# Optimization experiments

Hardware: AMD Instinct MI355X
Metric: run time of the kernel (lower is better)

The kernel has to match this reference:

```python
import jax, jax.numpy as jnp
import numpy as np

B, N, C = 64, 197, 768
H = 12
D = C // H
SCALE = D ** -0.5
TAU = 5.0
THRESHOLD = 0.6
NEG_INF = float('-inf')


def setup_inputs() -> dict:
    key = jax.random.key(0)
    ks = jax.random.split(key, 10)
    def gumbel(k, shape):
        # -log(Exponential) == standard Gumbel noise, matches torch exponential_().log()
        e = jax.random.exponential(k, shape, dtype=jnp.float32)
        return -jnp.log(e + 1e-10)
    s = 0.02
    return {
        'x': jax.random.normal(ks[0], (B, N, C), dtype=jnp.float32),
        'g1': gumbel(ks[1], (B, N - 1, 1)),
        'g2': gumbel(ks[2], (B, N - 1, 1)),
        'Wq': jax.random.normal(ks[3], (C, C), dtype=jnp.float32) * s,
        'Wk': jax.random.normal(ks[4], (C, C), dtype=jnp.float32) * s,
        'Wv': jax.random.normal(ks[5], (C, C), dtype=jnp.float32) * s,
        'Wp': jax.random.normal(ks[6], (C, C), dtype=jnp.float32) * s,
        'bp': jnp.zeros((C,), dtype=jnp.float32),
        'Wm': jax.random.normal(ks[7], (1, C), dtype=jnp.float32) * s,
        'bm': jnp.zeros((1,), dtype=jnp.float32),
    }


def reference(x, g1, g2, Wq, Wk, Wv, Wp, bp, Wm, bm):
    b, n, c = x.shape
    # QKV projections (qkv_bias=False), reshape to (B, H, N, D)
    q = (x @ Wq.T).reshape(b, n, H, D).transpose(0, 2, 1, 3)
    k = (x @ Wk.T).reshape(b, n, H, D).transpose(0, 2, 1, 3)
    v = (x @ Wv.T).reshape(b, n, H, D).transpose(0, 2, 1, 3)

    attn_pre = jnp.einsum('bhnd,bhmd->bhnm', q, k) * SCALE  # (B,H,N,N)

    # SimpleTokenSelect: gumbel-sigmoid gating on non-CLS tokens (training=True, hard=True)
    logits = x[:, 1:] @ Wm.T + bm                       # (B, N-1, 1)
    y_soft = jax.nn.sigmoid((logits + g1 - g2) / TAU)
    y_hard = (y_soft > THRESHOLD).astype(y_soft.dtype)
    ts = y_hard - jax.lax.stop_gradient(y_soft) + y_soft  # straight-through
    ts = jnp.concatenate([jnp.ones((b, 1, 1), dtype=ts.dtype), ts], axis=1)[..., 0]  # (B, N)

    # attention policy = outer product of token gates, detached (ada_token_detach_attn)
    policy = jax.lax.stop_gradient(jnp.einsum('bn,bm->bnm', ts, ts))[:, None]  # (B,1,N,N)

    # pre-softmax masking: zero gated scores, -inf off-diagonal entries of gated rows
    eye = jnp.eye(n, dtype=attn_pre.dtype)
    neg_mask = jnp.where(1.0 - policy - eye > 0, NEG_INF, 0.0)
    attn = jax.nn.softmax(attn_pre * policy + neg_mask, axis=-1)

    out = jnp.einsum('bhnm,bhmd->bhnd', attn, v)        # (B,H,N,D)
    out = out.transpose(0, 2, 1, 3).reshape(b, n, c)
    out = out @ Wp.T + bp                                # proj (dropout p=0)
    return out
```

## Files before the change

kernel.cpp:

```cpp
#include <hip/hip_runtime.h>
#include <hip/hip_bf16.h>
#include <cstdint>

typedef unsigned short u16;
typedef __attribute__((ext_vector_type(8))) short bf16x8;
typedef __attribute__((ext_vector_type(4))) float f32x4;

#define NB 64
#define NN 197
#define NC 768
#define NH 12
#define ND 64
#define NM (NB*NN)
#define CAP 96
#define NT 24
#define SELR 6144
#define MSELT 48
#define ASZ ((size_t)NM*NC)
#define WSZ ((size_t)NC*NC)
#define SELSZ2 ((size_t)SELR*NC)

__device__ __forceinline__ u16 f2bf(float f) {
  uint32_t u = __float_as_uint(f);
  u += 0x7fffu + ((u >> 16) & 1u);
  return (u16)(u >> 16);
}

__device__ __forceinline__ void gl_lds16(const u16* g, u16* l) {
  __builtin_amdgcn_global_load_lds(
      (const __attribute__((address_space(1))) void*)g,
      (__attribute__((address_space(3))) void*)l, 16, 0, 0);
}

#define GATEB 3152
#define WBLK 576
#define TRBLK 144
__global__ __launch_bounds__(256) void k1_prep(const float* __restrict__ x,
    const float* __restrict__ g1, const float* __restrict__ g2,
    const float* __restrict__ Wm, const float* __restrict__ bm,
    const float* __restrict__ wq, const float* __restrict__ wk,
    const float* __restrict__ wv, const float* __restrict__ wp,
    u16* __restrict__ xb, u16* __restrict__ wqb, u16* __restrict__ wkb,
    u16* __restrict__ wvb, u16* __restrict__ wpb, u16* __restrict__ wvt,
    float* __restrict__ ts) {
  __shared__ u16 T[64][72];
  int bid = blockIdx.x, tid = threadIdx.x;

  if (bid < GATEB) {
    int wave = tid >> 6, lane = tid & 63;
    int wid = bid * 4 + wave;
    int b = wid / NN, n = wid % NN;
    const float* xr = x + (size_t)wid * NC;
    u16* xbr = xb + (size_t)wid * NC;
    double acc = 0.0;
    #pragma unroll
    for (int i = 0; i < 3; ++i) {
      float4 f = *(const float4*)(xr + lane * 4 + 256 * i);
      float4 w = *(const float4*)(Wm + lane * 4 + 256 * i);
      acc += (double)f.x * w.x + (double)f.y * w.y
           + (double)f.z * w.z + (double)f.w * w.w;
      ushort4 o;
      o.x = f2bf(f.x); o.y = f2bf(f.y); o.z = f2bf(f.z); o.w = f2bf(f.w);
      *(ushort4*)(xbr + lane * 4 + 256 * i) = o;
    }
    #pragma unroll
    for (int off = 32; off; off >>= 1) acc += __shfl_down(acc, off);
    float o = 1.0f;
    if (n != 0) {
      double z = (acc + (double)bm[0] + (double)g1[b*(NN-1) + n - 1]
                                      - (double)g2[b*(NN-1) + n - 1]) / 5.0;
      o = (z > 0.4054651081081643820) ? 1.0f : 0.0f;
    }
    if (lane == 0) ts[wid] = o;
    return;
  }
  bid -= GATEB;
  if (bid < 4*WBLK) {
    int seg = bid / WBLK;
    int i = (bid - seg * WBLK) * 256 + tid;
    const float* src; u16* dst;
    if (seg == 0)      { src = wq; dst = wqb; }
    else if (seg == 1) { src = wk; dst = wkb; }
    else if (seg == 2) { src = wv; dst = wvb; }
    else               { src = wp; dst = wpb; }
    float4 f = ((const float4*)src)[i];
    ushort4 o;
    o.x = f2bf(f.x); o.y = f2bf(f.y); o.z = f2bf(f.z); o.w = f2bf(f.w);
    ((ushort4*)dst)[i] = o;
    return;
  }
  bid -= 4*WBLK;
  {
    int bx = bid % 12, by = bid / 12;
    int j0 = by * 64, k0 = bx * 64;
    #pragma unroll
    for (int g = 0; g < 4; ++g) {
      int r = g * 16 + (tid >> 4);
      int c4 = (tid & 15) * 4;
      float4 f = *(const float4*)(wv + (size_t)(j0 + r) * NC + k0 + c4);
      T[c4 + 0][r] = f2bf(f.x);
      T[c4 + 1][r] = f2bf(f.y);
      T[c4 + 2][r] = f2bf(f.z);
      T[c4 + 3][r] = f2bf(f.w);
    }
    __syncthreads();
    #pragma unroll
    for (int g = 0; g < 4; ++g) {
      int r = g * 16 + (tid >> 4);
      int c4 = (tid & 15) * 4;
      ushort4 o = *(ushort4*)&T[r][c4];
      *(ushort4*)(wvt + (size_t)(k0 + r) * NC + j0 + c4) = o;
    }
  }
}

__global__ __launch_bounds__(1024) void ck_compact(const float* __restrict__ ts,
    int* __restrict__ cnt, int* __restrict__ boff, int* __restrict__ gidx) {
  __shared__ unsigned long long masks[NB][4];
  __shared__ int scnt[NB];
  __shared__ int soff[NB + 1];
  int tid = threadIdx.x, lane = tid & 63, wave = tid >> 6;

  #pragma unroll
  for (int p = 0; p < 4; ++p) {
    int b = wave * 4 + p;
    int count = 0;
    #pragma unroll
    for (int c = 0; c < 4; ++c) {
      int t = c * 64 + lane;
      bool sel = (t < NN) && (ts[b * NN + t] > 0.5f);
      unsigned long long m = __ballot(sel);
      if (lane == 0) masks[b][c] = m;
      count += __popcll(m);
    }
    if (lane == 0) scnt[b] = count < CAP ? count : CAP;
  }
  __syncthreads();

  if (wave == 0) {
    int acc = 0;
    for (int i = 0; i < NB; ++i) {
      int v = scnt[i];
      if (i < lane) acc += v;
    }
    soff[lane] = acc;
    if (lane == 63) soff[NB] = acc + scnt[63];
  }
  __syncthreads();

  #pragma unroll
  for (int p = 0; p < 4; ++p) {
    int b = wave * 4 + p;
    int base = soff[b];
    int cc = scnt[b];
    int prior = 0;
    #pragma unroll
    for (int c = 0; c < 4; ++c) {
      unsigned long long m = masks[b][c];
      int t = c * 64 + lane;
      bool sel = ((m >> lane) & 1ull) != 0;
      int within = __popcll(m & ((lane == 0) ? 0ull : (~0ull >> (64 - lane))));
      int pos = prior + within;
      if (sel && pos < cc) gidx[base + pos] = b * NN + t;
      prior += __popcll(m);
    }
  }
  if (tid < NB) { cnt[tid] = scnt[tid]; boff[tid] = soff[tid]; }
  if (tid == NB) boff[NB] = soff[NB];
  __syncthreads();
  int total = soff[NB];
  for (int i = total + tid; i < SELR; i += 1024) gidx[i] = 0;
}

__global__ __launch_bounds__(256) void k2_wvp_qkv(const u16* __restrict__ xb,
    const u16* __restrict__ wq3, const u16* __restrict__ wpb,
    const u16* __restrict__ wvt, u16* __restrict__ wvpb,
    u16* __restrict__ sel3, const int* __restrict__ boff,
    const int* __restrict__ gidx) {
  alignas(16) __shared__ u16 SA[128][32];
  alignas(16) __shared__ u16 SB[128][32];
  int bid = blockIdx.x;
  int tid = threadIdx.x, lane = tid & 63, wave = tid >> 6;
  int lr = lane & 15, lg = lane >> 4, lk = lg * 8;
  int wr = (wave >> 1) * 64, wc = (wave & 1) * 64;

  int id0 = (wave*2 + 0) * 64 + lane, id1 = (wave*2 + 1) * 64 + lane;
  const u16 *baseA0, *baseA1, *baseB0, *baseB1;
  bool isSel = (bid < MSELT * 18);
  int m0, n0, total = 0, z = 0;
  if (isSel) {
    int mt = bid / 18, r18 = bid % 18;
    z = r18 / 6; int y = r18 % 6;
    total = boff[NB];
    m0 = mt * 128;
    if (m0 >= total) return;
    n0 = y * 128;
    const u16* W = wq3 + (size_t)z * WSZ;
    baseA0 = xb + (size_t)gidx[m0 + (id0 >> 2)] * NC + (id0 & 3) * 8;
    baseA1 = xb + (size_t)gidx[m0 + (id1 >> 2)] * NC + (id1 & 3) * 8;
    baseB0 = W + (size_t)(n0 + (id0 >> 2)) * NC + (id0 & 3) * 8;
    baseB1 = W + (size_t)(n0 + (id1 >> 2)) * NC + (id1 & 3) * 8;
  } else {
    int wb = bid - MSELT * 18;
    m0 = (wb / 6) * 128; n0 = (wb % 6) * 128;
    baseA0 = wpb + (size_t)(m0 + (id0 >> 2)) * NC + (id0 & 3) * 8;
    baseA1 = wpb + (size_t)(m0 + (id1 >> 2)) * NC + (id1 & 3) * 8;
    baseB0 = wvt + (size_t)(n0 + (id0 >> 2)) * NC + (id0 & 3) * 8;
    baseB1 = wvt + (size_t)(n0 + (id1 >> 2)) * NC + (id1 & 3) * 8;
  }
  u16* dA0 = &SA[0][0] + (size_t)(wave*2 + 0) * 512;
  u16* dA1 = &SA[0][0] + (size_t)(wave*2 + 1) * 512;
  u16* dB0 = &SB[0][0] + (size_t)(wave*2 + 0) * 512;
  u16* dB1 = &SB[0][0] + (size_t)(wave*2 + 1) * 512;

  f32x4 acc[4][4];
  #pragma unroll
  for (int i = 0; i < 4; ++i)
    #pragma unroll
    for (int j = 0; j < 4; ++j) acc[i][j] = (f32x4){0.f,0.f,0.f,0.f};

  for (int k0 = 0; k0 < NC; k0 += 32) {
    gl_lds16(baseA0 + k0, dA0);
    gl_lds16(baseA1 + k0, dA1);
    gl_lds16(baseB0 + k0, dB0);
    gl_lds16(baseB1 + k0, dB1);
    __syncthreads();
    bf16x8 af[4], bfr[4];
    #pragma unroll
    for (int f = 0; f < 4; ++f) {
      af[f]  = *(const bf16x8*)(&SA[wr + f*16 + lr][lk]);
      bfr[f] = *(const bf16x8*)(&SB[wc + f*16 + lr][lk]);
    }
    #pragma unroll
    for (int i = 0; i < 4; ++i)
      #pragma unroll
      for (int j = 0; j < 4; ++j)
        acc[i][j] = __builtin_amdgcn_mfma_f32_16x16x32_bf16(af[i], bfr[j], acc[i][j], 0, 0, 0);
    __syncthreads();
  }

  if (isSel) {
    u16* o = sel3 + (size_t)z * SELSZ2;
    #pragma unroll
    for (int i = 0; i < 4; ++i) {
      int rbase = m0 + wr + i*16 + 4*lg;
      #pragma unroll
      for (int j = 0; j < 4; ++j) {
        int col = n0 + wc + j*16 + lr;
        #pragma unroll
        for (int r = 0; r < 4; ++r) {
          int row = rbase + r;
          if (row < total)
            o[(size_t)row * NC + col] = f2bf(acc[i][j][r]);
        }
      }
    }
  } else {
    #pragma unroll
    for (int i = 0; i < 4; ++i)
      #pragma unroll
      for (int j = 0; j < 4; ++j)
        #pragma unroll
        for (int r = 0; r < 4; ++r)
          wvpb[(size_t)(m0 + wr + i*16 + 4*lg + r) * NC + n0 + wc + j*16 + lr] =
              f2bf(acc[i][j][r]);
  }
}

#define DTOT 594
#define DN1 378
#define DN2 (DTOT-DN1)
__global__ __launch_bounds__(256) void k3_dense_attn(const u16* __restrict__ xb,
    const u16* __restrict__ wvpb, const u16* __restrict__ qsel,
    const u16* __restrict__ ksel, const u16* __restrict__ vsel,
    u16* __restrict__ zsel, const float* __restrict__ ts,
    const float* __restrict__ bp, float* __restrict__ out,
    const int* __restrict__ cnt, const int* __restrict__ boff) {
  alignas(16) __shared__ u16 LDSU[64*232];
  int bid = blockIdx.x;
  int tid = threadIdx.x, lane = tid & 63, wave = tid >> 6;
  int lr = lane & 15, lg = lane >> 4;

  if (bid < DN1) {
    u16 (*SA)[32] = reinterpret_cast<u16(*)[32]>(&LDSU[0]);
    u16 (*SB)[32] = reinterpret_cast<u16(*)[32]>(&LDSU[4096]);
    int lk = lg * 8;
    int wr = (wave >> 1) * 64, wc = (wave & 1) * 64;
    int d = bid;
    int xcd = d & 7, loc = d >> 3;
    int wgid = (xcd < 2 ? xcd * 75 : 150 + (xcd - 2) * 74) + loc;
    int m0 = (wgid / 6) * 128, n0 = (wgid % 6) * 128;

    int id0 = (wave*2 + 0) * 64 + lane, id1 = (wave*2 + 1) * 64 + lane;
    const u16* baseA0 = xb + (size_t)(m0 + (id0 >> 2)) * NC + (id0 & 3) * 8;
    const u16* baseA1 = xb + (size_t)(m0 + (id1 >> 2)) * NC + (id1 & 3) * 8;
    const u16* baseB0 = wvpb + (size_t)(n0 + (id0 >> 2)) * NC + (id0 & 3) * 8;
    const u16* baseB1 = wvpb + (size_t)(n0 + (id1 >> 2)) * NC + (id1 & 3) * 8;
    u16* dA0 = &SA[0][0] + (size_t)(wave*2 + 0) * 512;
    u16* dA1 = &SA[0][0] + (size_t)(wave*2 + 1) * 512;
    u16* dB0 = &SB[0][0] + (size_t)(wave*2 + 0) * 512;
    u16* dB1 = &SB[0][0] + (size_t)(wave*2 + 1) * 512;

    f32x4 acc[4][4];
    #pragma unroll
    for (int i = 0; i < 4; ++i)
      #pragma unroll
      for (int j = 0; j < 4; ++j) acc[i][j] = (f32x4){0.f,0.f,0.f,0.f};

    for (int k0 = 0; k0 < NC; k0 += 32) {
      gl_lds16(baseA0 + k0, dA0);
      gl_lds16(baseA1 + k0, dA1);
      gl_lds16(baseB0 + k0, dB0);
      gl_lds16(baseB1 + k0, dB1);
      __syncthreads();
      bf16x8 af[4], bfr[4];
      #pragma unroll
      for (int f = 0; f < 4; ++f) {
        af[f]  = *(const bf16x8*)(&SA[wr + f*16 + lr][lk]);
        bfr[f] = *(const bf16x8*)(&SB[wc + f*16 + lr][lk]);
      }
      #pragma unroll
      for (int i = 0; i < 4; ++i)
        #pragma unroll
        for (int j = 0; j < 4; ++j)
          acc[i][j] = __builtin_amdgcn_mfma_f32_16x16x32_bf16(af[i], bfr[j], acc[i][j], 0, 0, 0);
      __syncthreads();
    }
    #pragma unroll
    for (int i = 0; i < 4; ++i) {
      int rbase = m0 + wr + i*16 + 4*lg;
      #pragma unroll
      for (int j = 0; j < 4; ++j) {
        int col = n0 + wc + j*16 + lr;
        #pragma unroll
        for (int r = 0; r < 4; ++r) {
          int row = rbase + r;
          if (row < NM && ts[row] < 0.5f)
            out[(size_t)row * NC + col] = acc[i][j][r] + bp[col];
        }
      }
    }
    return;
  }

  u16 (*Vt)[232] = reinterpret_cast<u16(*)[232]>(&LDSU[0]);
  int bh = bid - DN1;
  int b = bh / NH, h = bh % NH;
  int cntb = cnt[b];
  int boffb = boff[b];
  const size_t qbase = (size_t)boffb * NC + (size_t)h * ND;

  for (int id = tid; id < cntb * 8; id += 256) {
    int i = id >> 3, c8 = (id & 7) * 8;
    int4 val = *(const int4*)(vsel + qbase + (size_t)i * NC + c8);
    u16 tmp[8];
    *(int4*)tmp = val;
    #pragma unroll
    for (int e = 0; e < 8; ++e) Vt[c8 + e][i] = tmp[e];
  }
  for (int id = tid; id < 64 * 32; id += 256)
    Vt[id >> 5][cntb + (id & 31)] = 0;
  __syncthreads();

  int nchunk = (cntb + 15) >> 4;
  int mtmax  = nchunk;
  int mcmax  = (cntb + 31) >> 5;
  int idx0 = (((lane & 15) | ((lane & 16) << 1))) << 2;
  int idx1 = idx0 + 64;

  for (int qc = wave; qc < nchunk; qc += 4) {
    const u16* qp = qsel + qbase + (size_t)(qc * 16 + lr) * NC + lg * 8;
    bf16x8 qf0 = *(const bf16x8*)(qp);
    bf16x8 qf1 = *(const bf16x8*)(qp + 32);

    f32x4 s[6];
    #pragma unroll
    for (int mt = 0; mt < 6; ++mt) s[mt] = (f32x4){0.f,0.f,0.f,0.f};
    #pragma unroll
    for (int mt = 0; mt < 6; ++mt) {
      if (mt < mtmax) {
        const u16* kp = ksel + qbase + (size_t)(mt * 16 + lr) * NC + lg * 8;
        bf16x8 kf0 = *(const bf16x8*)(kp);
        bf16x8 kf1 = *(const bf16x8*)(kp + 32);
        f32x4 a = (f32x4){0.f,0.f,0.f,0.f};
        a = __builtin_amdgcn_mfma_f32_16x16x32_bf16(kf0, qf0, a, 0, 0, 0);
        a = __builtin_amdgcn_mfma_f32_16x16x32_bf16(kf1, qf1, a, 0, 0, 0);
        s[mt] = a;
      }
    }

    float mx = -3e38f;
    #pragma unroll
    for (int mt = 0; mt < 6; ++mt)
      #pragma unroll
      for (int jj = 0; jj < 4; ++jj) {
        int mm = mt*16 + 4*lg + jj;
        float val = (mm < cntb) ? s[mt][jj] * 0.125f : -1e30f;
        s[mt][jj] = val;
        mx = fmaxf(mx, val);
      }
    mx = fmaxf(mx, __shfl_xor(mx, 16));
    mx = fmaxf(mx, __shfl_xor(mx, 32));
    float sum = 0.f;
    #pragma unroll
    for (int mt = 0; mt < 6; ++mt)
      #pragma unroll
      for (int jj = 0; jj < 4; ++jj) {
        float pv = __expf(s[mt][jj] - mx);
        s[mt][jj] = pv;
        sum += pv;
      }
    sum += __shfl_xor(sum, 16);
    sum += __shfl_xor(sum, 32);
    float inv = 1.0f / sum;

    uint32_t u[6][2];
    #pragma unroll
    for (int mt = 0; mt < 6; ++mt) {
      u[mt][0] = ((uint32_t)f2bf(s[mt][1]*inv) << 16) | f2bf(s[mt][0]*inv);
      u[mt][1] = ((uint32_t)f2bf(s[mt][3]*inv) << 16) | f2bf(s[mt][2]*inv);
    }

    f32x4 oacc[4];
    #pragma unroll
    for (int dt = 0; dt < 4; ++dt) oacc[dt] = (f32x4){0.f,0.f,0.f,0.f};
    #pragma unroll
    for (int mc = 0; mc < 3; ++mc) {
      if (mc < mcmax) {
        uint32_t a0 = (uint32_t)__builtin_amdgcn_ds_bpermute(idx0, (int)u[2*mc][0]);
        uint32_t b0 = (uint32_t)__builtin_amdgcn_ds_bpermute(idx0, (int)u[2*mc+1][0]);
        uint32_t a1 = (uint32_t)__builtin_amdgcn_ds_bpermute(idx0, (int)u[2*mc][1]);
        uint32_t b1 = (uint32_t)__builtin_amdgcn_ds_bpermute(idx0, (int)u[2*mc+1][1]);
        uint32_t a2 = (uint32_t)__builtin_amdgcn_ds_bpermute(idx1, (int)u[2*mc][0]);
        uint32_t b2 = (uint32_t)__builtin_amdgcn_ds_bpermute(idx1, (int)u[2*mc+1][0]);
        uint32_t a3 = (uint32_t)__builtin_amdgcn_ds_bpermute(idx1, (int)u[2*mc][1]);
        uint32_t b3 = (uint32_t)__builtin_amdgcn_ds_bpermute(idx1, (int)u[2*mc+1][1]);
        bool hi = (lg >= 2);
        union { uint32_t w[4]; bf16x8 v; } pu;
        pu.w[0] = hi ? b0 : a0;
        pu.w[1] = hi ? b1 : a1;
        pu.w[2] = hi ? b2 : a2;
        pu.w[3] = hi ? b3 : a3;
        bf16x8 pa = pu.v;
        #pragma unroll
        for (int dt = 0; dt < 4; ++dt) {
          bf16x8 vf = *(const bf16x8*)(&Vt[dt*16 + lr][mc*32 + lg*8]);
          oacc[dt] = __builtin_amdgcn_mfma_f32_16x16x32_bf16(pa, vf, oacc[dt], 0, 0, 0);
        }
      }
    }

    #pragma unroll
    for (int r = 0; r < 4; ++r) {
      int nloc = qc*16 + 4*lg + r;
      if (nloc < cntb) {
        u16* op = zsel + qbase + (size_t)nloc * NC + lr;
        #pragma unroll
        for (int dt = 0; dt < 4; ++dt)
          op[dt*16] = f2bf(oacc[dt][r]);
      }
    }
  }
}

#define PJBLK (MSELT*6)
__global__ __launch_bounds__(256) void k4_out(const u16* __restrict__ xb,
    const u16* __restrict__ wvpb, const u16* __restrict__ zsel,
    const u16* __restrict__ wpb, const float* __restrict__ ts,
    const float* __restrict__ bp, float* __restrict__ out,
    const int* __restrict__ boff, const int* __restrict__ gidx) {
  alignas(16) __shared__ u16 SA[128][32];
  alignas(16) __shared__ u16 SB[128][32];
  int bid = blockIdx.x;
  int tid = threadIdx.x, lane = tid & 63, wave = tid >> 6;
  int lr = lane & 15, lg = lane >> 4, lk = lg * 8;
  int wr = (wave >> 1) * 64, wc = (wave & 1) * 64;

  const u16* Abase; const u16* Bbase;
  int m0, n0, total = 0;
  bool dense = (bid >= PJBLK);
  if (dense) {
    int d = DN1 + (bid - PJBLK);
    int xcd = d & 7, loc = d >> 3;
    int wgid = (xcd < 2 ? xcd * 75 : 150 + (xcd - 2) * 74) + loc;
    m0 = (wgid / 6) * 128;
    n0 = (wgid % 6) * 128;
    Abase = xb; Bbase = wvpb;
  } else {
    int mt = bid / 6, y = bid % 6;
    total = boff[NB];
    m0 = mt * 128;
    if (m0 >= total) return;
    n0 = y * 128;
    Abase = zsel; Bbase = wpb;
  }

  int id0 = (wave*2 + 0) * 64 + lane, id1 = (wave*2 + 1) * 64 + lane;
  const u16* baseA0 = Abase + (size_t)(m0 + (id0 >> 2)) * NC + (id0 & 3) * 8;
  const u16* baseA1 = Abase + (size_t)(m0 + (id1 >> 2)) * NC + (id1 & 3) * 8;
  const u16* baseB0 = Bbase + (size_t)(n0 + (id0 >> 2)) * NC + (id0 & 3) * 8;
  const u16* baseB1 = Bbase + (size_t)(n0 + (id1 >> 2)) * NC + (id1 & 3) * 8;
  u16* dA0 = &SA[0][0] + (size_t)(wave*2 + 0) * 512;
  u16* dA1 = &SA[0][0] + (size_t)(wave*2 + 1) * 512;
  u16* dB0 = &SB[0][0] + (size_t)(wave*2 + 0) * 512;
  u16* dB1 = &SB[0][0] + (size_t)(wave*2 + 1) * 512;

  f32x4 acc[4][4];
  #pragma unroll
  for (int i = 0; i < 4; ++i)
    #pragma unroll
    for (int j = 0; j < 4; ++j) acc[i][j] = (f32x4){0.f,0.f,0.f,0.f};

  for (int k0 = 0; k0 < NC; k0 += 32) {
    gl_lds16(baseA0 + k0, dA0);
    gl_lds16(baseA1 + k0, dA1);
    gl_lds16(baseB0 + k0, dB0);
    gl_lds16(baseB1 + k0, dB1);
    __syncthreads();
    bf16x8 af[4], bfr[4];
    #pragma unroll
    for (int f = 0; f < 4; ++f) {
      af[f]  = *(const bf16x8*)(&SA[wr + f*16 + lr][lk]);
      bfr[f] = *(const bf16x8*)(&SB[wc + f*16 + lr][lk]);
    }
    #pragma unroll
    for (int i = 0; i < 4; ++i)
      #pragma unroll
      for (int j = 0; j < 4; ++j)
        acc[i][j] = __builtin_amdgcn_mfma_f32_16x16x32_bf16(af[i], bfr[j], acc[i][j], 0, 0, 0);
    __syncthreads();
  }

  if (dense) {
    #pragma unroll
    for (int i = 0; i < 4; ++i) {
      int rbase = m0 + wr + i*16 + 4*lg;
      #pragma unroll
      for (int j = 0; j < 4; ++j) {
        int col = n0 + wc + j*16 + lr;
        #pragma unroll
        for (int r = 0; r < 4; ++r) {
          int row = rbase + r;
          if (row < NM && ts[row] < 0.5f)
            out[(size_t)row * NC + col] = acc[i][j][r] + bp[col];
        }
      }
    }
  } else {
    #pragma unroll
    for (int i = 0; i < 4; ++i) {
      int rbase = m0 + wr + i*16 + 4*lg;
      #pragma unroll
      for (int j = 0; j < 4; ++j) {
        int col = n0 + wc + j*16 + lr;
        #pragma unroll
        for (int r = 0; r < 4; ++r) {
          int row = rbase + r;
          if (row < total) {
            int grow = gidx[row];
            out[(size_t)grow * NC + col] = acc[i][j][r] + bp[col];
          }
        }
      }
    }
  }
}

extern "C" void kernel_launch(void* const* d_in, const int* in_sizes, int n_in,
                              void* d_out, int out_size, void* d_ws, size_t ws_size,
                              hipStream_t stream) {
  const float* x  = (const float*)d_in[0];
  const float* g1 = (const float*)d_in[1];
  const float* g2 = (const float*)d_in[2];
  const float* Wq = (const float*)d_in[3];
  const float* Wk = (const float*)d_in[4];
  const float* Wv = (const float*)d_in[5];
  const float* Wp = (const float*)d_in[6];
  const float* bp = (const float*)d_in[7];
  const float* Wm = (const float*)d_in[8];
  const float* bm = (const float*)d_in[9];
  float* out = (float*)d_out;

  const size_t act_sz = ASZ * 2;
  const size_t w_sz   = WSZ * 2;
  const size_t sel_sz = SELSZ2 * 2;
  size_t need = act_sz + 4*sel_sz + 6*w_sz + (size_t)NM*4
              + (size_t)(NB+1)*4 + (size_t)NB*4 + (size_t)SELR*4 + 256;
  if (ws_size < need) return;

  char* p = (char*)d_ws;
  u16* xb   = (u16*)p; p += act_sz;
  u16* qsel = (u16*)p; p += sel_sz;
  u16* ksel = (u16*)p; p += sel_sz;
  u16* vsel = (u16*)p; p += sel_sz;
  u16* zsel = (u16*)p; p += sel_sz;
  u16* wqb  = (u16*)p; p += w_sz;
  u16* wkb  = (u16*)p; p += w_sz;
  u16* wvb  = (u16*)p; p += w_sz;
  u16* wpb  = (u16*)p; p += w_sz;
  u16* wvtb = (u16*)p; p += w_sz;
  u16* wvpb = (u16*)p; p += w_sz;
  float* ts = (float*)p; p += (size_t)NM*4;
  int* cnt  = (int*)p;  p += (size_t)NB*4;
  int* boff = (int*)p;  p += (size_t)(NB+1)*4;
  int* gidx = (int*)p;
  (void)wkb; (void)wvb;

  k1_prep<<<dim3(GATEB + 4*WBLK + TRBLK), 256, 0, stream>>>(
      x, g1, g2, Wm, bm, Wq, Wk, Wv, Wp,
      xb, wqb, wkb, wvb, wpb, wvtb, ts);

  ck_compact<<<dim3(1), 1024, 0, stream>>>(ts, cnt, boff, gidx);

  k2_wvp_qkv<<<dim3(MSELT*18 + 36), 256, 0, stream>>>(
      xb, wqb, wpb, wvtb, wvpb, qsel, boff, gidx);

  k3_dense_attn<<<dim3(DN1 + NB*NH), 256, 0, stream>>>(
      xb, wvpb, qsel, ksel, vsel, zsel, ts, bp, out, cnt, boff);

  k4_out<<<dim3(PJBLK + DN2), 256, 0, stream>>>(
      xb, wvpb, zsel, wpb, ts, bp, out, boff, gidx);
}
```

Measured before the change: 113.0 us.

## Switch GEMMs to 256x128 tiles with 512-thread blocks via shared template body

Unifies the four GEMM paths into one templated body that computes 256x128 output tiles with 8 waves per block, replacing the 128x128 tiles with 4 waves. Each block now loads a taller A tile against the same B tile, halving B reloads per output and halving the block count. The dense/split partition counts and XCD remapping are retuned, and the attention part now runs with 8 waves per block. Fewer, larger blocks may reduce occupancy and worsen wave quantization on the CUs.

```diff
diff --git a/kernel.cpp b/kernel.cpp
--- a/kernel.cpp
+++ b/kernel.cpp
@@ -15,7 +15,7 @@
 #define CAP 96
 #define NT 24
 #define SELR 6144
-#define MSELT 48
+#define MT256 24
 #define ASZ ((size_t)NM*NC)
 #define WSZ ((size_t)NC*NC)
 #define SELSZ2 ((size_t)SELR*NC)
@@ -30,6 +30,80 @@
   __builtin_amdgcn_global_load_lds(
       (const __attribute__((address_space(1))) void*)g,
       (__attribute__((address_space(3))) void*)l, 16, 0, 0);
+}
+
+template<int GATHER, int OUTM>
+__device__ __forceinline__ void gemm256_body(
+    const u16* __restrict__ A, const u16* __restrict__ B,
+    u16* __restrict__ obf, float* __restrict__ of32,
+    const float* __restrict__ bias, const float* __restrict__ ts,
+    const int* __restrict__ gidx, int m0, int n0, int bound,
+    u16* SAf, u16* SBf) {
+  int tid = threadIdx.x, lane = tid & 63, wave = tid >> 6;
+  int lr = lane & 15, lg = lane >> 4, lk = lg * 8;
+  int wr = (wave >> 1) * 64, wc = (wave & 1) * 64;
+  int idA0 = tid, idA1 = 512 + tid, idB = tid;
+  const u16 *baseA0, *baseA1;
+  if (GATHER) {
+    baseA0 = A + (size_t)gidx[m0 + (idA0 >> 2)] * NC + (idA0 & 3) * 8;
+    baseA1 = A + (size_t)gidx[m0 + (idA1 >> 2)] * NC + (idA1 & 3) * 8;
+  } else {
+    baseA0 = A + (size_t)(m0 + (idA0 >> 2)) * NC + (idA0 & 3) * 8;
+    baseA1 = A + (size_t)(m0 + (idA1 >> 2)) * NC + (idA1 & 3) * 8;
+  }
+  const u16* baseB0 = B + (size_t)(n0 + (idB >> 2)) * NC + (idB & 3) * 8;
+  u16* dA0 = SAf + (size_t)idA0 * 8;
+  u16* dA1 = SAf + (size_t)idA1 * 8;
+  u16* dB0 = SBf + (size_t)idB * 8;
+
+  f32x4 acc[4][4];
+  #pragma unroll
+  for (int i = 0; i < 4; ++i)
+    #pragma unroll
+    for (int j = 0; j < 4; ++j) acc[i][j] = (f32x4){0.f,0.f,0.f,0.f};
+
+  for (int k0 = 0; k0 < NC; k0 += 32) {
+    gl_lds16(baseA0 + k0, dA0);
+    gl_lds16(baseA1 + k0, dA1);
+    gl_lds16(baseB0 + k0, dB0);
+    __syncthreads();
+    bf16x8 af[4], bfr[4];
+    #pragma unroll
+    for (int f = 0; f < 4; ++f) {
+      af[f]  = *(const bf16x8*)(SAf + (size_t)(wr + f*16 + lr) * 32 + lk);
+      bfr[f] = *(const bf16x8*)(SBf + (size_t)(wc + f*16 + lr) * 32 + lk);
+    }
+    #pragma unroll
+    for (int i = 0; i < 4; ++i)
+      #pragma unroll
+      for (int j = 0; j < 4; ++j)
+        acc[i][j] = __builtin_amdgcn_mfma_f32_16x16x32_bf16(af[i], bfr[j], acc[i][j], 0, 0, 0);
+    __syncthreads();
+  }
+
+  #pragma unroll
+  for (int i = 0; i < 4; ++i) {
+    int rbase = m0 + wr + i*16 + 4*lg;
+    #pragma unroll
+    for (int j = 0; j < 4; ++j) {
+      int col = n0 + wc + j*16 + lr;
+      #pragma unroll
+      for (int r = 0; r < 4; ++r) {
+        int row = rbase + r;
+        if (OUTM == 0) {
+          if (row < bound) obf[(size_t)row * NC + col] = f2bf(acc[i][j][r]);
+        } else if (OUTM == 1) {
+          if (row < NM && ts[row] < 0.5f)
+            of32[(size_t)row * NC + col] = acc[i][j][r] + bias[col];
+        } else {
+          if (row < bound) {
+            int grow = gidx[row];
+            of32[(size_t)grow * NC + col] = acc[i][j][r] + bias[col];
+          }
+        }
+      }
+    }
+  }
 }
 
 #define GATEB 3152
@@ -172,185 +246,62 @@
   for (int i = total + tid; i < SELR; i += 1024) gidx[i] = 0;
 }
 
-__global__ __launch_bounds__(256) void k2_wvp_qkv(const u16* __restrict__ xb,
+__global__ __launch_bounds__(512) void k2_wvp_qkv(const u16* __restrict__ xb,
     const u16* __restrict__ wq3, const u16* __restrict__ wpb,
     const u16* __restrict__ wvt, u16* __restrict__ wvpb,
     u16* __restrict__ sel3, const int* __restrict__ boff,
     const int* __restrict__ gidx) {
-  alignas(16) __shared__ u16 SA[128][32];
+  alignas(16) __shared__ u16 SA[256][32];
   alignas(16) __shared__ u16 SB[128][32];
   int bid = blockIdx.x;
-  int tid = threadIdx.x, lane = tid & 63, wave = tid >> 6;
-  int lr = lane & 15, lg = lane >> 4, lk = lg * 8;
-  int wr = (wave >> 1) * 64, wc = (wave & 1) * 64;
-
-  int id0 = (wave*2 + 0) * 64 + lane, id1 = (wave*2 + 1) * 64 + lane;
-  const u16 *baseA0, *baseA1, *baseB0, *baseB1;
-  bool isSel = (bid < MSELT * 18);
-  int m0, n0, total = 0, z = 0;
-  if (isSel) {
+  if (bid < MT256 * 18) {
     int mt = bid / 18, r18 = bid % 18;
-    z = r18 / 6; int y = r18 % 6;
-    total = boff[NB];
-    m0 = mt * 128;
+    int z = r18 / 6, y = r18 % 6;
+    int total = boff[NB];
+    int m0 = mt * 256;
     if (m0 >= total) return;
-    n0 = y * 128;
-    const u16* W = wq3 + (size_t)z * WSZ;
-    baseA0 = xb + (size_t)gidx[m0 + (id0 >> 2)] * NC + (id0 & 3) * 8;
-    baseA1 = xb + (size_t)gidx[m0 + (id1 >> 2)] * NC + (id1 & 3) * 8;
-    baseB0 = W + (size_t)(n0 + (id0 >> 2)) * NC + (id0 & 3) * 8;
-    baseB1 = W + (size_t)(n0 + (id1 >> 2)) * NC + (id1 & 3) * 8;
+    gemm256_body<1, 0>(xb, wq3 + (size_t)z * WSZ,
+                       sel3 + (size_t)z * SELSZ2, nullptr, nullptr, nullptr,
+                       gidx, m0, y * 128, total, &SA[0][0], &SB[0][0]);
   } else {
-    int wb = bid - MSELT * 18;
-    m0 = (wb / 6) * 128; n0 = (wb % 6) * 128;
-    baseA0 = wpb + (size_t)(m0 + (id0 >> 2)) * NC + (id0 & 3) * 8;
-    baseA1 = wpb + (size_t)(m0 + (id1 >> 2)) * NC + (id1 & 3) * 8;
-    baseB0 = wvt + (size_t)(n0 + (id0 >> 2)) * NC + (id0 & 3) * 8;
-    baseB1 = wvt + (size_t)(n0 + (id1 >> 2)) * NC + (id1 & 3) * 8;
-  }
-  u16* dA0 = &SA[0][0] + (size_t)(wave*2 + 0) * 512;
-  u16* dA1 = &SA[0][0] + (size_t)(wave*2 + 1) * 512;
-  u16* dB0 = &SB[0][0] + (size_t)(wave*2 + 0) * 512;
-  u16* dB1 = &SB[0][0] + (size_t)(wave*2 + 1) * 512;
-
-  f32x4 acc[4][4];
-  #pragma unroll
-  for (int i = 0; i < 4; ++i)
-    #pragma unroll
-    for (int j = 0; j < 4; ++j) acc[i][j] = (f32x4){0.f,0.f,0.f,0.f};
-
-  for (int k0 = 0; k0 < NC; k0 += 32) {
-    gl_lds16(baseA0 + k0, dA0);
-    gl_lds16(baseA1 + k0, dA1);
-    gl_lds16(baseB0 + k0, dB0);
-    gl_lds16(baseB1 + k0, dB1);
-    __syncthreads();
-    bf16x8 af[4], bfr[4];
-    #pragma unroll
-    for (int f = 0; f < 4; ++f) {
-      af[f]  = *(const bf16x8*)(&SA[wr + f*16 + lr][lk]);
-      bfr[f] = *(const bf16x8*)(&SB[wc + f*16 + lr][lk]);
-    }
-    #pragma unroll
-    for (int i = 0; i < 4; ++i)
-      #pragma unroll
-      for (int j = 0; j < 4; ++j)
-        acc[i][j] = __builtin_amdgcn_mfma_f32_16x16x32_bf16(af[i], bfr[j], acc[i][j], 0, 0, 0);
-    __syncthreads();
-  }
-
-  if (isSel) {
-    u16* o = sel3 + (size_t)z * SELSZ2;
-    #pragma unroll
-    for (int i = 0; i < 4; ++i) {
-      int rbase = m0 + wr + i*16 + 4*lg;
-      #pragma unroll
-      for (int j = 0; j < 4; ++j) {
-        int col = n0 + wc + j*16 + lr;
-        #pragma unroll
-        for (int r = 0; r < 4; ++r) {
-          int row = rbase + r;
-          if (row < total)
-            o[(size_t)row * NC + col] = f2bf(acc[i][j][r]);
-        }
-      }
-    }
-  } else {
-    #pragma unroll
-    for (int i = 0; i < 4; ++i)
-      #pragma unroll
-      for (int j = 0; j < 4; ++j)
-        #pragma unroll
-        for (int r = 0; r < 4; ++r)
-          wvpb[(size_t)(m0 + wr + i*16 + 4*lg + r) * NC + n0 + wc + j*16 + lr] =
-              f2bf(acc[i][j][r]);
-  }
-}
-
-#define DTOT 594
-#define DN1 378
+    int wb = bid - MT256 * 18;
+    gemm256_body<0, 0>(wpb, wvt, wvpb, nullptr, nullptr, nullptr,
+                       nullptr, (wb / 6) * 256, (wb % 6) * 128, NC,
+                       &SA[0][0], &SB[0][0]);
+  }
+}
+
+#define DTOT 300
+#define DN1 192
 #define DN2 (DTOT-DN1)
-__global__ __launch_bounds__(256) void k3_dense_attn(const u16* __restrict__ xb,
+__global__ __launch_bounds__(512) void k3_dense_attn(const u16* __restrict__ xb,
     const u16* __restrict__ wvpb, const u16* __restrict__ qsel,
     const u16* __restrict__ ksel, const u16* __restrict__ vsel,
     u16* __restrict__ zsel, const float* __restrict__ ts,
     const float* __restrict__ bp, float* __restrict__ out,
     const int* __restrict__ cnt, const int* __restrict__ boff) {
-  alignas(16) __shared__ u16 LDSU[64*232];
+  alignas(16) __shared__ u16 LDSU[12288];
   int bid = blockIdx.x;
   int tid = threadIdx.x, lane = tid & 63, wave = tid >> 6;
   int lr = lane & 15, lg = lane >> 4;
 
   if (bid < DN1) {
-    u16 (*SA)[32] = reinterpret_cast<u16(*)[32]>(&LDSU[0]);
-    u16 (*SB)[32] = reinterpret_cast<u16(*)[32]>(&LDSU[4096]);
-    int lk = lg * 8;
-    int wr = (wave >> 1) * 64, wc = (wave & 1) * 64;
-    int d = bid;
-    int xcd = d & 7, loc = d >> 3;
-    int wgid = (xcd < 2 ? xcd * 75 : 150 + (xcd - 2) * 74) + loc;
-    int m0 = (wgid / 6) * 128, n0 = (wgid % 6) * 128;
-
-    int id0 = (wave*2 + 0) * 64 + lane, id1 = (wave*2 + 1) * 64 + lane;
-    const u16* baseA0 = xb + (size_t)(m0 + (id0 >> 2)) * NC + (id0 & 3) * 8;
-    const u16* baseA1 = xb + (size_t)(m0 + (id1 >> 2)) * NC + (id1 & 3) * 8;
-    const u16* baseB0 = wvpb + (size_t)(n0 + (id0 >> 2)) * NC + (id0 & 3) * 8;
-    const u16* baseB1 = wvpb + (size_t)(n0 + (id1 >> 2)) * NC + (id1 & 3) * 8;
-    u16* dA0 = &SA[0][0] + (size_t)(wave*2 + 0) * 512;
-    u16* dA1 = &SA[0][0] + (size_t)(wave*2 + 1) * 512;
-    u16* dB0 = &SB[0][0] + (size_t)(wave*2 + 0) * 512;
-    u16* dB1 = &SB[0][0] + (size_t)(wave*2 + 1) * 512;
-
-    f32x4 acc[4][4];
-    #pragma unroll
-    for (int i = 0; i < 4; ++i)
-      #pragma unroll
-      for (int j = 0; j < 4; ++j) acc[i][j] = (f32x4){0.f,0.f,0.f,0.f};
-
-    for (int k0 = 0; k0 < NC; k0 += 32) {
-      gl_lds16(baseA0 + k0, dA0);
-      gl_lds16(baseA1 + k0, dA1);
-      gl_lds16(baseB0 + k0, dB0);
-      gl_lds16(baseB1 + k0, dB1);
-      __syncthreads();
-      bf16x8 af[4], bfr[4];
-      #pragma unroll
-      for (int f = 0; f < 4; ++f) {
-        af[f]  = *(const bf16x8*)(&SA[wr + f*16 + lr][lk]);
-        bfr[f] = *(const bf16x8*)(&SB[wc + f*16 + lr][lk]);
-      }
-      #pragma unroll
-      for (int i = 0; i < 4; ++i)
-        #pragma unroll
-        for (int j = 0; j < 4; ++j)
-          acc[i][j] = __builtin_amdgcn_mfma_f32_16x16x32_bf16(af[i], bfr[j], acc[i][j], 0, 0, 0);
-      __syncthreads();
-    }
-    #pragma unroll
-    for (int i = 0; i < 4; ++i) {
-      int rbase = m0 + wr + i*16 + 4*lg;
-      #pragma unroll
-      for (int j = 0; j < 4; ++j) {
-        int col = n0 + wc + j*16 + lr;
-        #pragma unroll
-        for (int r = 0; r < 4; ++r) {
-          int row = rbase + r;
-          if (row < NM && ts[row] < 0.5f)
-            out[(size_t)row * NC + col] = acc[i][j][r] + bp[col];
-        }
-      }
-    }
+    int xcd = bid & 7, loc = bid >> 3;
+    int wgid = (xcd < 4 ? xcd * 38 : 152 + (xcd - 4) * 37) + loc;
+    gemm256_body<0, 1>(xb, wvpb, nullptr, out, bp, ts, nullptr,
+                       (wgid / 6) * 256, (wgid % 6) * 128, NM,
+                       &LDSU[0], &LDSU[8192]);
     return;
   }
 
-  u16 (*Vt)[232] = reinterpret_cast<u16(*)[232]>(&LDSU[0]);
+  u16 (*Vt)[136] = reinterpret_cast<u16(*)[136]>(&LDSU[0]);
   int bh = bid - DN1;
   int b = bh / NH, h = bh % NH;
   int cntb = cnt[b];
   int boffb = boff[b];
   const size_t qbase = (size_t)boffb * NC + (size_t)h * ND;
 
-  for (int id = tid; id < cntb * 8; id += 256) {
+  for (int id = tid; id < cntb * 8; id += 512) {
     int i = id >> 3, c8 = (id & 7) * 8;
     int4 val = *(const int4*)(vsel + qbase + (size_t)i * NC + c8);
     u16 tmp[8];
@@ -358,7 +309,7 @@
     #pragma unroll
     for (int e = 0; e < 8; ++e) Vt[c8 + e][i] = tmp[e];
   }
-  for (int id = tid; id < 64 * 32; id += 256)
+  for (int id = tid; id < 64 * 32; id += 512)
     Vt[id >> 5][cntb + (id & 31)] = 0;
   __syncthreads();
 
@@ -368,7 +319,7 @@
   int idx0 = (((lane & 15) | ((lane & 16) << 1))) << 2;
   int idx1 = idx0 + 64;
 
-  for (int qc = wave; qc < nchunk; qc += 4) {
+  for (int qc = wave; qc < nchunk; qc += 8) {
     const u16* qp = qsel + qbase + (size_t)(qc * 16 + lr) * NC + lg * 8;
     bf16x8 qf0 = *(const bf16x8*)(qp);
     bf16x8 qf1 = *(const bf16x8*)(qp + 32);
@@ -463,106 +414,29 @@
   }
 }
 
-#define PJBLK (MSELT*6)
-__global__ __launch_bounds__(256) void k4_out(const u16* __restrict__ xb,
+#define PJBLK (MT256*6)
+__global__ __launch_bounds__(512) void k4_out(const u16* __restrict__ xb,
     const u16* __restrict__ wvpb, const u16* __restrict__ zsel,
     const u16* __restrict__ wpb, const float* __restrict__ ts,
     const float* __restrict__ bp, float* __restrict__ out,
     const int* __restrict__ boff, const int* __restrict__ gidx) {
-  alignas(16) __shared__ u16 SA[128][32];
+  alignas(16) __shared__ u16 SA[256][32];
   alignas(16) __shared__ u16 SB[128][32];
   int bid = blockIdx.x;
-  int tid = threadIdx.x, lane = tid & 63, wave = tid >> 6;
-  int lr = lane & 15, lg = lane >> 4, lk = lg * 8;
-  int wr = (wave >> 1) * 64, wc = (wave & 1) * 64;
-
-  const u16* Abase; const u16* Bbase;
-  int m0, n0, total = 0;
-  bool dense = (bid >= PJBLK);
-  if (dense) {
+  if (bid < PJBLK) {
+    int mt = bid / 6, y = bid % 6;
+    int total = boff[NB];
+    int m0 = mt * 256;
+    if (m0 >= total) return;
+    gemm256_body<0, 2>(zsel, wpb, nullptr, out, bp, nullptr,
+                       gidx, m0, y * 128, total, &SA[0][0], &SB[0][0]);
+  } else {
     int d = DN1 + (bid - PJBLK);
     int xcd = d & 7, loc = d >> 3;
-    int wgid = (xcd < 2 ? xcd * 75 : 150 + (xcd - 2) * 74) + loc;
-    m0 = (wgid / 6) * 128;
-    n0 = (wgid % 6) * 128;
-    Abase = xb; Bbase = wvpb;
-  } else {
-    int mt = bid / 6, y = bid % 6;
-    total = boff[NB];
-    m0 = mt * 128;
-    if (m0 >= total) return;
-    n0 = y * 128;
-    Abase = zsel; Bbase = wpb;
-  }
-
-  int id0 = (wave*2 + 0) * 64 + lane, id1 = (wave*2 + 1) * 64 + lane;
-  const u16* baseA0 = Abase + (size_t)(m0 + (id0 >> 2)) * NC + (id0 & 3) * 8;
-  const u16* baseA1 = Abase + (size_t)(m0 + (id1 >> 2)) * NC + (id1 & 3) * 8;
-  const u16* baseB0 = Bbase + (size_t)(n0 + (id0 >> 2)) * NC + (id0 & 3) * 8;
-  const u16* baseB1 = Bbase + (size_t)(n0 + (id1 >> 2)) * NC + (id1 & 3) * 8;
-  u16* dA0 = &SA[0][0] + (size_t)(wave*2 + 0) * 512;
-  u16* dA1 = &SA[0][0] + (size_t)(wave*2 + 1) * 512;
-  u16* dB0 = &SB[0][0] + (size_t)(wave*2 + 0) * 512;
-  u16* dB1 = &SB[0][0] + (size_t)(wave*2 + 1) * 512;
-
-  f32x4 acc[4][4];
-  #pragma unroll
-  for (int i = 0; i < 4; ++i)
-    #pragma unroll
-    for (int j = 0; j < 4; ++j) acc[i][j] = (f32x4){0.f,0.f,0.f,0.f};
-
-  for (int k0 = 0; k0 < NC; k0 += 32) {
-    gl_lds16(baseA0 + k0, dA0);
-    gl_lds16(baseA1 + k0, dA1);
-    gl_lds16(baseB0 + k0, dB0);
-    gl_lds16(baseB1 + k0, dB1);
-    __syncthreads();
-    bf16x8 af[4], bfr[4];
-    #pragma unroll
-    for (int f = 0; f < 4; ++f) {
-      af[f]  = *(const bf16x8*)(&SA[wr + f*16 + lr][lk]);
-      bfr[f] = *(const bf16x8*)(&SB[wc + f*16 + lr][lk]);
-    }
-    #pragma unroll
-    for (int i = 0; i < 4; ++i)
-      #pragma unroll
-      for (int j = 0; j < 4; ++j)
-        acc[i][j] = __builtin_amdgcn_mfma_f32_16x16x32_bf16(af[i], bfr[j], acc[i][j], 0, 0, 0);
-    __syncthreads();
-  }
-
-  if (dense) {
-    #pragma unroll
-    for (int i = 0; i < 4; ++i) {
-      int rbase = m0 + wr + i*16 + 4*lg;
-      #pragma unroll
-      for (int j = 0; j < 4; ++j) {
-        int col = n0 + wc + j*16 + lr;
-        #pragma unroll
-        for (int r = 0; r < 4; ++r) {
-          int row = rbase + r;
-          if (row < NM && ts[row] < 0.5f)
-            out[(size_t)row * NC + col] = acc[i][j][r] + bp[col];
-        }
-      }
-    }
-  } else {
-    #pragma unroll
-    for (int i = 0; i < 4; ++i) {
-      int rbase = m0 + wr + i*16 + 4*lg;
-      #pragma unroll
-      for (int j = 0; j < 4; ++j) {
-        int col = n0 + wc + j*16 + lr;
-        #pragma unroll
-        for (int r = 0; r < 4; ++r) {
-          int row = rbase + r;
-          if (row < total) {
-            int grow = gidx[row];
-            out[(size_t)grow * NC + col] = acc[i][j][r] + bp[col];
-          }
-        }
-      }
-    }
+    int wgid = (xcd < 4 ? xcd * 38 : 152 + (xcd - 4) * 37) + loc;
+    gemm256_body<0, 1>(xb, wvpb, nullptr, out, bp, ts, nullptr,
+                       (wgid / 6) * 256, (wgid % 6) * 128, NM,
+                       &SA[0][0], &SB[0][0]);
   }
 }
 
@@ -612,12 +486,12 @@
 
   ck_compact<<<dim3(1), 1024, 0, stream>>>(ts, cnt, boff, gidx);
 
-  k2_wvp_qkv<<<dim3(MSELT*18 + 36), 256, 0, stream>>>(
+  k2_wvp_qkv<<<dim3(MT256*18 + 18), 512, 0, stream>>>(
       xb, wqb, wpb, wvtb, wvpb, qsel, boff, gidx);
 
-  k3_dense_attn<<<dim3(DN1 + NB*NH), 256, 0, stream>>>(
+  k3_dense_attn<<<dim3(DN1 + NB*NH), 512, 0, stream>>>(
       xb, wvpb, qsel, ksel, vsel, zsel, ts, bp, out, cnt, boff);
 
-  k4_out<<<dim3(PJBLK + DN2), 256, 0, stream>>>(
+  k4_out<<<dim3(PJBLK + DN2), 512, 0, stream>>>(
       xb, wvpb, zsel, wpb, ts, bp, out, boff, gidx);
 }
```

Result: slower. 122.2 us (+8.2%).
